# Performance work log

Hardware: AMD Instinct MI355X
Metric: run time of the kernel (lower is better)

The kernel has to match this reference:

```python
import jax, jax.numpy as jnp
import numpy as np

TMPL = jnp.array([[-0.9, 1.2, 0.0], [0.0, 0.0, 0.0], [2.5, 0.0, 0.0]], dtype=jnp.float32)
EYE3 = jnp.eye(3, dtype=jnp.float32)


def _normalize(v, eps=1e-12):
    n = jnp.maximum(jnp.linalg.norm(v, axis=-1, keepdims=True), eps)
    return v / n


def _layer_norm(x, g, b, eps=1e-5):
    mu = jnp.mean(x, axis=-1, keepdims=True)
    var = jnp.var(x, axis=-1, keepdims=True)
    return (x - mu) * jax.lax.rsqrt(var + eps) * g + b


def _build_frames(coords, mask):
    P = coords[..., 0, :]
    C4p = coords[..., 1, :]
    N = coords[..., 2, :]
    e1 = _normalize(N - C4p)
    u = P - C4p
    e2 = _normalize(u - jnp.sum(u * e1, axis=-1, keepdims=True) * e1)
    e3 = jnp.cross(e1, e2)
    R = jnp.stack([e1, e2, e3], axis=-1)  # (B,L,3,3), columns = e1,e2,e3
    pad = ~mask
    R = jnp.where(pad[..., None, None], EYE3, R)
    return R, C4p


def _invariants(R, t):
    # dt[b,i,j] = t[b,j] - t[b,i]
    dt = t[:, None, :, :] - t[:, :, None, :]  # (B,L,L,3)
    # local frame of i: Ri^T @ dt
    dt_l = jnp.einsum('bixk,bijx->bijk', R, dt)  # (B,L,L,3)
    dist = jnp.maximum(jnp.linalg.norm(dt, axis=-1, keepdims=True), 1e-4)
    log_d = jnp.log(dist)
    # trace(Ri^T Rj)
    trace = jnp.einsum('bixk,bjxk->bij', R, R)[..., None]  # (B,L,L,1)
    cos_a = jnp.clip((trace - 1.0) / 2.0, -1.0, 1.0)
    return jnp.concatenate([dist, dt_l, trace, cos_a, log_d], axis=-1)  # (B,L,L,7)


def _skew(v):
    z = jnp.zeros_like(v[..., 0])
    x, y, zz = v[..., 0], v[..., 1], v[..., 2]
    r0 = jnp.stack([z, -zz, y], axis=-1)
    r1 = jnp.stack([zz, z, -x], axis=-1)
    r2 = jnp.stack([-y, x, z], axis=-1)
    return jnp.stack([r0, r1, r2], axis=-2)


def _apply_frame_update(R, t, dr, dt, mask):
    mf = mask.astype(R.dtype)[..., None]
    dr = dr * mf
    dt = dt * mf
    angle = jnp.maximum(jnp.linalg.norm(dr, axis=-1, keepdims=True), 1e-8)
    axis = dr / angle
    cos_a = jnp.cos(angle)[..., None]
    sin_a = jnp.sin(angle)[..., None]
    K = _skew(axis)
    outer = axis[..., :, None] * axis[..., None, :]
    R_delta = cos_a * EYE3 + sin_a * K + (1.0 - cos_a) * outer
    R_new = R_delta @ R
    t_new = t + jnp.einsum('blxy,bly->blx', R, dt)
    return R_new, t_new


def _reconstruct_atoms(R, t):
    # coords[b,l,a,:] = t[b,l] + R[b,l] @ TMPL[a]
    d = jnp.einsum('blxy,ay->blax', R, TMPL)
    return t[:, :, None, :] + d


def _gelu(x):
    return jax.nn.gelu(x, approximate=False)


def _forward(h, coords, mask, pair_w1, pair_b1, pair_w2, pair_b2, gw_w, gw_b, ga_w, ga_b,
             ln_g, ln_b, fh_ln_g, fh_ln_b, fh_w1, fh_b1, fh_w2, fh_b2):
    R, t = _build_frames(coords, mask)
    n_steps = pair_w1.shape[0]
    coords_list = []
    for s in range(n_steps):
        inv = _invariants(R, t)  # (B,L,L,7)
        pm = (mask[:, None, :] & mask[:, :, None]).astype(h.dtype)  # (B,L,L)
        msg = _gelu(inv @ pair_w1[s] + pair_b1[s]) @ pair_w2[s] + pair_b2[s]  # (B,L,L,D)
        n_v = jnp.maximum(jnp.sum(pm, axis=2, keepdims=True), 1.0)  # (B,L,1)
        agg = jnp.sum(msg * pm[..., None], axis=2) / n_v  # (B,L,D)
        h_s = _layer_norm(h, ln_g[s], ln_b[s])
        cat = jnp.concatenate([h_s, agg], axis=-1)
        g = cat @ gw_w[s] + gw_b[s]
        a = jax.nn.sigmoid(cat @ ga_w[s] + ga_b[s])
        h_aug = h + a * g
        fh = _gelu(_layer_norm(h_aug, fh_ln_g, fh_ln_b) @ fh_w1 + fh_b1) @ fh_w2 + fh_b2
        delta_r, delta_t = fh[..., :3], fh[..., 3:]
        R, t = _apply_frame_update(R, t, delta_r, delta_t, mask)
        coords_list.append(_reconstruct_atoms(R, t))
    return coords_list[-1], jnp.stack(coords_list, axis=0)


def setup_inputs() -> dict:
    key = jax.random.key(0)
    B, L, D, H, S = 2, 512, 256, 64, 4
    ks = jax.random.split(key, 16)
    w = lambda k, shp: jax.random.normal(k, shp, dtype=jnp.float32) * 0.02
    return {
        'h': jax.random.normal(ks[0], (B, L, D), dtype=jnp.float32),
        'coords': jax.random.normal(ks[1], (B, L, 3, 3), dtype=jnp.float32),
        'mask': jnp.ones((B, L), dtype=bool),
        'pair_w1': w(ks[2], (S, 7, H)), 'pair_b1': jnp.zeros((S, H), jnp.float32),
        'pair_w2': w(ks[3], (S, H, D)), 'pair_b2': jnp.zeros((S, D), jnp.float32),
        'gw_w': w(ks[4], (S, 2 * D, D)), 'gw_b': jnp.zeros((S, D), jnp.float32),
        'ga_w': w(ks[5], (S, 2 * D, D)), 'ga_b': jnp.zeros((S, D), jnp.float32),
        'ln_g': jnp.ones((S, D), jnp.float32), 'ln_b': jnp.zeros((S, D), jnp.float32),
        'fh_ln_g': jnp.ones((D,), jnp.float32), 'fh_ln_b': jnp.zeros((D,), jnp.float32),
        'fh_w1': w(ks[6], (D, D // 2)), 'fh_b1': jnp.zeros((D // 2,), jnp.float32),
        'fh_w2': w(ks[7], (D // 2, 6)), 'fh_b2': jnp.zeros((6,), jnp.float32),
    }


def reference(h, coords, mask, pair_w1, pair_b1, pair_w2, pair_b2, gw_w, gw_b, ga_w, ga_b,
              ln_g, ln_b, fh_ln_g, fh_ln_b, fh_w1, fh_b1, fh_w2, fh_b2):
    return _forward(h, coords, mask, pair_w1, pair_b1, pair_w2, pair_b2, gw_w, gw_b,
                    ga_w, ga_b, ln_g, ln_b, fh_ln_g, fh_ln_b, fh_w1, fh_b1, fh_w2, fh_b2)
```

## Files before the change

kernel.cpp:

```cpp
#include <hip/hip_runtime.h>
#include <math.h>

#define BB 2
#define LL 512
#define DD 256
#define HH 64
#define NSTEP 4
#define NTOK (BB * LL)

__device__ __forceinline__ float geluf(float x) {
    return 0.5f * x * (1.0f + erff(x * 0.70710678118654752f));
}
__device__ __forceinline__ float sigmoidf_(float x) {
    return 1.0f / (1.0f + expf(-x));
}
__device__ __forceinline__ float gelu_fast(float x) {
    float u = 0.70710678118654752f * x;
    float a = fabsf(u);
    float t = __builtin_amdgcn_rcpf(fmaf(0.3275911f, a, 1.0f));
    float p = fmaf(t, 1.061405429f, -1.453152027f);
    p = fmaf(t, p, 1.421413741f);
    p = fmaf(t, p, -0.284496736f);
    p = fmaf(t, p, 0.254829592f);
    p = p * t;
    float e = __expf(-u * u);
    float erfa = fmaf(-p, e, 1.0f);
    float erfu = copysignf(erfa, u);
    return 0.5f * x * (1.0f + erfu);
}
#define F4C(v, j) ((j) == 0 ? (v).x : (j) == 1 ? (v).y : (j) == 2 ? (v).z : (v).w)

__global__ void build_frames_kernel(const float* __restrict__ coords,
                                    float* __restrict__ Rg, float* __restrict__ tg) {
    int idx = blockIdx.x * blockDim.x + threadIdx.x;
    if (idx >= NTOK) return;
    const float* c = coords + idx * 9;
    float Px = c[0], Py = c[1], Pz = c[2];
    float Cx = c[3], Cy = c[4], Cz = c[5];
    float Nx = c[6], Ny = c[7], Nz = c[8];
    float e1x = Nx - Cx, e1y = Ny - Cy, e1z = Nz - Cz;
    float n1 = fmaxf(sqrtf(e1x * e1x + e1y * e1y + e1z * e1z), 1e-12f);
    e1x /= n1; e1y /= n1; e1z /= n1;
    float ux = Px - Cx, uy = Py - Cy, uz = Pz - Cz;
    float du = ux * e1x + uy * e1y + uz * e1z;
    float e2x = ux - du * e1x, e2y = uy - du * e1y, e2z = uz - du * e1z;
    float n2 = fmaxf(sqrtf(e2x * e2x + e2y * e2y + e2z * e2z), 1e-12f);
    e2x /= n2; e2y /= n2; e2z /= n2;
    float e3x = e1y * e2z - e1z * e2y;
    float e3y = e1z * e2x - e1x * e2z;
    float e3z = e1x * e2y - e1y * e2x;
    float* Rp = Rg + idx * 9;
    Rp[0] = e1x; Rp[1] = e2x; Rp[2] = e3x;
    Rp[3] = e1y; Rp[4] = e2y; Rp[5] = e3y;
    Rp[6] = e1z; Rp[7] = e2z; Rp[8] = e3z;
    tg[idx * 3 + 0] = Cx; tg[idx * 3 + 1] = Cy; tg[idx * 3 + 2] = Cz;
}

__global__ __launch_bounds__(256) void ln4_kernel(
        const float* __restrict__ hIn,
        const float* __restrict__ lng, const float* __restrict__ lnb,
        float* __restrict__ hln) {
    __shared__ float redsh[8];
    const int i = blockIdx.x;
    const int tid = threadIdx.x;
    const int wv = tid >> 6, lane = tid & 63;
    float hv = hIn[(size_t)i * DD + tid];
    float s1 = hv, s2 = hv * hv;
#pragma unroll
    for (int off = 32; off > 0; off >>= 1) {
        s1 += __shfl_xor(s1, off);
        s2 += __shfl_xor(s2, off);
    }
    if (lane == 0) { redsh[wv * 2] = s1; redsh[wv * 2 + 1] = s2; }
    __syncthreads();
    float S1 = redsh[0] + redsh[2] + redsh[4] + redsh[6];
    float S2 = redsh[1] + redsh[3] + redsh[5] + redsh[7];
    float mu = S1 * (1.0f / DD);
    float var = S2 * (1.0f / DD) - mu * mu;
    float rs = rsqrtf(var + 1e-5f);
    float hn = (hv - mu) * rs;
#pragma unroll
    for (int s = 0; s < NSTEP; s++)
        hln[((size_t)s * NTOK + i) * DD + tid] = hn * lng[s * DD + tid] + lnb[s * DD + tid];
}

__global__ void fold_w1_kernel(const float* __restrict__ w1all,
                               const float* __restrict__ b1all,
                               float* __restrict__ w1f) {
    const int s = blockIdx.x;
    const int h = threadIdx.x;
    const float* w1 = w1all + s * 7 * HH;
    float w5 = w1[5 * HH + h];
    float* o = w1f + ((size_t)s * HH + h) * 8;
    o[0] = w1[0 * HH + h];
    o[1] = w1[1 * HH + h];
    o[2] = w1[2 * HH + h];
    o[3] = w1[3 * HH + h];
    o[4] = fmaf(0.5f, w5, w1[4 * HH + h]);
    o[5] = w1[6 * HH + h];
    o[6] = fmaf(-0.5f, w5, b1all[s * HH + h]);
    o[7] = 0.0f;
}

__global__ __launch_bounds__(256) void fuse_w_kernel(
        const float* __restrict__ w2all, const float* __restrict__ b2all,
        const float* __restrict__ gww, const float* __restrict__ gaw,
        const float* __restrict__ gwb, const float* __restrict__ gab,
        float* __restrict__ Wfus, float* __restrict__ biasGA) {
    __shared__ float bsh[256 * 17];

    const int bid = blockIdx.x;
    const int s = bid >> 5;
    const int gate = (bid >> 4) & 1;
    const int ct = bid & 15;
    const int c0 = ct * 16;
    const int tid = threadIdx.x;

    const float* Wb = (gate ? gaw : gww) + (size_t)s * 2 * DD * DD + (size_t)DD * DD;
    {
        const float* src = Wb + (size_t)tid * DD + c0;
        float4 a0 = *(const float4*)(src + 0);
        float4 a1 = *(const float4*)(src + 4);
        float4 a2 = *(const float4*)(src + 8);
        float4 a3 = *(const float4*)(src + 12);
        float* dst = &bsh[tid * 17];
        dst[0] = a0.x; dst[1] = a0.y; dst[2] = a0.z; dst[3] = a0.w;
        dst[4] = a1.x; dst[5] = a1.y; dst[6] = a1.z; dst[7] = a1.w;
        dst[8] = a2.x; dst[9] = a2.y; dst[10] = a2.z; dst[11] = a2.w;
        dst[12] = a3.x; dst[13] = a3.y; dst[14] = a3.z; dst[15] = a3.w;
    }
    __syncthreads();

    const int r = tid & 63;
    const int cg = tid >> 6;
    const float* w2p = w2all + (size_t)s * HH * DD + (size_t)r * DD;
    float4 acc = {0.f, 0.f, 0.f, 0.f};
#pragma unroll 4
    for (int k4 = 0; k4 < 64; k4++) {
        float4 wv = *(const float4*)(w2p + k4 * 4);
#pragma unroll
        for (int j = 0; j < 4; j++) {
            const float* bp = &bsh[(k4 * 4 + j) * 17 + cg * 4];
            float w = F4C(wv, j);
            acc.x = fmaf(w, bp[0], acc.x);
            acc.y = fmaf(w, bp[1], acc.y);
            acc.z = fmaf(w, bp[2], acc.z);
            acc.w = fmaf(w, bp[3], acc.w);
        }
    }
    acc.x *= (1.0f / 512.0f); acc.y *= (1.0f / 512.0f);
    acc.z *= (1.0f / 512.0f); acc.w *= (1.0f / 512.0f);
    *(float4*)&Wfus[((size_t)s * HH + r) * 512 + gate * 256 + c0 + cg * 4] = acc;

    if (tid < 16) {
        const float* b2 = b2all + s * DD;
        float a = 0.0f;
#pragma unroll 4
        for (int m = 0; m < 256; m++) a = fmaf(b2[m], bsh[m * 17 + tid], a);
        const float* gb = (gate ? gab : gwb) + s * DD;
        biasGA[(size_t)s * 512 + gate * 256 + c0 + tid] = a + gb[c0 + tid];
    }
}

__global__ __launch_bounds__(256) void gpreh_kernel(
        const float* __restrict__ hln,
        const float* __restrict__ gww, const float* __restrict__ gaw,
        const float* __restrict__ biasGA,
        float* __restrict__ gpreH) {
    __shared__ float hsh[16 * DD];
    const int bid = blockIdx.x;
    const int s = bid >> 7;
    const int gate = (bid >> 6) & 1;
    const int mt = bid & 63;
    const int tid = threadIdx.x;

    const float* hsrc = hln + ((size_t)s * NTOK + mt * 16) * DD;
    for (int k = tid; k < 16 * DD; k += 256) hsh[k] = hsrc[k];
    __syncthreads();

    const float* W = (gate ? gaw : gww) + (size_t)s * 2 * DD * DD;
    float bias = biasGA[(size_t)s * 512 + gate * 256 + tid];
    float acc[16];
#pragma unroll
    for (int t = 0; t < 16; t++) acc[t] = bias;
#pragma unroll 4
    for (int k = 0; k < DD; k++) {
        float w = W[(size_t)k * DD + tid];
#pragma unroll
        for (int t = 0; t < 16; t++) acc[t] = fmaf(hsh[t * DD + k], w, acc[t]);
    }
    float* out = gpreH + ((size_t)s * NTOK + mt * 16) * 512 + gate * 256 + tid;
#pragma unroll
    for (int t = 0; t < 16; t++) out[(size_t)t * 512] = acc[t];
}

__global__ __launch_bounds__(256, 4) void mega_kernel(
        const float* __restrict__ Rin, const float* __restrict__ tin,
        float* __restrict__ Rout, float* __restrict__ tout,
        const float* __restrict__ w1fS,
        const float* __restrict__ WfusS, const float* __restrict__ gpreHS,
        const float* __restrict__ hIn,
        const float* __restrict__ fhlng, const float* __restrict__ fhlnb,
        const float* __restrict__ fhw1, const float* __restrict__ fhb1,
        const float* __restrict__ fhw2, const float* __restrict__ fhb2,
        float* __restrict__ outFinal, float* __restrict__ outStack, int s) {
    __shared__ float Rsh[LL * 9];
    __shared__ float tsh[LL * 3];
    __shared__ float feats[6][LL];
    __shared__ float asum[HH];
    __shared__ float ln2s[DD];
    __shared__ float fh1p[2 * 128];
    __shared__ float fh1s[128];
    __shared__ float partS[24];
    __shared__ float fhsh[6];
    __shared__ float redsh[8];

    const int i = blockIdx.x;
    const int b = i >> 9;
    const int l = i & (LL - 1);
    const int tid = threadIdx.x;
    const int g = tid >> 6;
    const int hh = tid & 63;

    const float* Rb = Rin + (size_t)b * LL * 9;
    const float* tb = tin + (size_t)b * LL * 3;
    for (int k = tid; k < LL * 9; k += 256) Rsh[k] = Rb[k];
    for (int k = tid; k < LL * 3; k += 256) tsh[k] = tb[k];
    __syncthreads();

    float Ri[9];
#pragma unroll
    for (int k = 0; k < 9; k++) Ri[k] = Rsh[l * 9 + k];
    const float tix = tsh[l * 3 + 0], tiy = tsh[l * 3 + 1], tiz = tsh[l * 3 + 2];

#pragma unroll
    for (int half = 0; half < 2; half++) {
        const int j = half * 256 + tid;
        float dx = tsh[j * 3 + 0] - tix;
        float dy = tsh[j * 3 + 1] - tiy;
        float dz = tsh[j * 3 + 2] - tiz;
        float dl0 = Ri[0] * dx + Ri[3] * dy + Ri[6] * dz;
        float dl1 = Ri[1] * dx + Ri[4] * dy + Ri[7] * dz;
        float dl2 = Ri[2] * dx + Ri[5] * dy + Ri[8] * dz;
        float dist = fmaxf(sqrtf(dx * dx + dy * dy + dz * dz), 1e-4f);
        float tr = 0.0f;
#pragma unroll
        for (int k = 0; k < 9; k++) tr = fmaf(Ri[k], Rsh[j * 9 + k], tr);
        feats[0][j] = dist;
        feats[1][j] = dl0;
        feats[2][j] = dl1;
        feats[3][j] = dl2;
        feats[4][j] = tr;
        feats[5][j] = __logf(dist);
    }
    __syncthreads();

    const int h0g = __builtin_amdgcn_readfirstlane(g) * 16;
#pragma unroll
    for (int hp = 0; hp < 2; hp++) {
        const float* wrow = w1fS + (size_t)(h0g + hp * 8) * 8;
        float acc0 = 0.f, acc1 = 0.f, acc2 = 0.f, acc3 = 0.f;
        float acc4 = 0.f, acc5 = 0.f, acc6 = 0.f, acc7 = 0.f;
        for (int c = 0; c < 8; c++) {
            const int j = c * 64 + hh;
            const float F0 = feats[0][j];
            const float F1 = feats[1][j];
            const float F2 = feats[2][j];
            const float F3 = feats[3][j];
            const float F4 = feats[4][j];
            const float F5 = feats[5][j];
#pragma unroll
            for (int k = 0; k < 8; k++) {
                const float* wr = wrow + k * 8;
                float x = wr[6];
                x = fmaf(F0, wr[0], x);
                x = fmaf(F1, wr[1], x);
                x = fmaf(F2, wr[2], x);
                x = fmaf(F3, wr[3], x);
                x = fmaf(F4, wr[4], x);
                x = fmaf(F5, wr[5], x);
                float gv = gelu_fast(x);
                if (k == 0) acc0 += gv;
                else if (k == 1) acc1 += gv;
                else if (k == 2) acc2 += gv;
                else if (k == 3) acc3 += gv;
                else if (k == 4) acc4 += gv;
                else if (k == 5) acc5 += gv;
                else if (k == 6) acc6 += gv;
                else acc7 += gv;
            }
        }
        float accs[8] = {acc0, acc1, acc2, acc3, acc4, acc5, acc6, acc7};
#pragma unroll
        for (int k = 0; k < 8; k++) {
            float v = accs[k];
#pragma unroll
            for (int off = 1; off < 64; off <<= 1) v += __shfl_xor(v, off);
            if (hh == k) asum[h0g + hp * 8 + k] = v;
        }
    }
    __syncthreads();

    float gpg = gpreHS[(size_t)i * 512 + tid];
    float gpa = gpreHS[(size_t)i * 512 + 256 + tid];
#pragma unroll 8
    for (int k = 0; k < HH; k++) {
        float av = asum[k];
        gpg = fmaf(av, WfusS[(size_t)k * 512 + tid], gpg);
        gpa = fmaf(av, WfusS[(size_t)k * 512 + 256 + tid], gpa);
    }
    float hv = hIn[(size_t)i * DD + tid];
    float haug = hv + sigmoidf_(gpa) * gpg;

    {
        float s1 = haug, s2 = haug * haug;
#pragma unroll
        for (int off = 32; off > 0; off >>= 1) {
            s1 += __shfl_xor(s1, off);
            s2 += __shfl_xor(s2, off);
        }
        if (hh == 0) { redsh[g * 2] = s1; redsh[g * 2 + 1] = s2; }
    }
    __syncthreads();
    {
        float S1 = redsh[0] + redsh[2] + redsh[4] + redsh[6];
        float S2 = redsh[1] + redsh[3] + redsh[5] + redsh[7];
        float mu = S1 * (1.0f / DD);
        float var = S2 * (1.0f / DD) - mu * mu;
        float rs = rsqrtf(var + 1e-5f);
        ln2s[tid] = (haug - mu) * rs * fhlng[tid] + fhlnb[tid];
    }
    __syncthreads();

    {
        const int col = tid & 127;
        const int kh = tid >> 7;
        float a = 0.0f;
        const float* wp = fhw1 + (size_t)(kh * 128) * 128 + col;
        const float* lp = &ln2s[kh * 128];
#pragma unroll 8
        for (int k = 0; k < 128; k++) a = fmaf(lp[k], wp[(size_t)k * 128], a);
        fh1p[kh * 128 + col] = a;
    }
    __syncthreads();
    if (tid < 128) fh1s[tid] = geluf(fh1p[tid] + fh1p[128 + tid] + fhb1[tid]);
    __syncthreads();

    if (tid < 24) {
        const int kq = tid / 6, m = tid % 6;
        float a = 0.0f;
#pragma unroll
        for (int j = 0; j < 32; j++) {
            int k = kq * 32 + j;
            a = fmaf(fh1s[k], fhw2[k * 6 + m], a);
        }
        partS[tid] = a;
    }
    __syncthreads();
    if (tid < 6)
        fhsh[tid] = partS[tid] + partS[6 + tid] + partS[12 + tid] + partS[18 + tid] + fhb2[tid];
    __syncthreads();

    if (tid == 0) {
        float R9[9], t3[3];
#pragma unroll
        for (int k = 0; k < 9; k++) R9[k] = Rsh[l * 9 + k];
        t3[0] = tix; t3[1] = tiy; t3[2] = tiz;
        float drx = fhsh[0], dry = fhsh[1], drz = fhsh[2];
        float dtx = fhsh[3], dty = fhsh[4], dtz = fhsh[5];
        float ang = fmaxf(sqrtf(drx * drx + dry * dry + drz * drz), 1e-8f);
        float ax = drx / ang, ay = dry / ang, az = drz / ang;
        float ca = cosf(ang), sa = sinf(ang), omc = 1.0f - ca;
        float Rd[9];
        Rd[0] = ca + omc * ax * ax;        Rd[1] = -sa * az + omc * ax * ay;  Rd[2] = sa * ay + omc * ax * az;
        Rd[3] = sa * az + omc * ay * ax;   Rd[4] = ca + omc * ay * ay;        Rd[5] = -sa * ax + omc * ay * az;
        Rd[6] = -sa * ay + omc * az * ax;  Rd[7] = sa * ax + omc * az * ay;   Rd[8] = ca + omc * az * az;
        float Rn[9];
#pragma unroll
        for (int x = 0; x < 3; x++)
#pragma unroll
            for (int y = 0; y < 3; y++)
                Rn[x * 3 + y] = Rd[x * 3 + 0] * R9[0 * 3 + y]
                              + Rd[x * 3 + 1] * R9[1 * 3 + y]
                              + Rd[x * 3 + 2] * R9[2 * 3 + y];
        float tn[3];
#pragma unroll
        for (int x = 0; x < 3; x++)
            tn[x] = t3[x] + R9[x * 3 + 0] * dtx + R9[x * 3 + 1] * dty + R9[x * 3 + 2] * dtz;
#pragma unroll
        for (int k = 0; k < 9; k++) Rout[(size_t)i * 9 + k] = Rn[k];
#pragma unroll
        for (int k = 0; k < 3; k++) tout[(size_t)i * 3 + k] = tn[k];
        float* os = outStack + ((size_t)s * NTOK + i) * 9;
        float av[9];
#pragma unroll
        for (int x = 0; x < 3; x++) {
            float r0 = Rn[x * 3 + 0], r1 = Rn[x * 3 + 1];
            av[0 * 3 + x] = tn[x] - 0.9f * r0 + 1.2f * r1;
            av[1 * 3 + x] = tn[x];
            av[2 * 3 + x] = tn[x] + 2.5f * r0;
        }
#pragma unroll
        for (int k = 0; k < 9; k++) os[k] = av[k];
        if (s == NSTEP - 1) {
            float* of = outFinal + (size_t)i * 9;
#pragma unroll
            for (int k = 0; k < 9; k++) of[k] = av[k];
        }
    }
}

extern "C" void kernel_launch(void* const* d_in, const int* in_sizes, int n_in,
                              void* d_out, int out_size, void* d_ws, size_t ws_size,
                              hipStream_t stream) {
    const float* h      = (const float*)d_in[0];
    const float* coords = (const float*)d_in[1];
    const float* pw1   = (const float*)d_in[3];
    const float* pb1   = (const float*)d_in[4];
    const float* pw2   = (const float*)d_in[5];
    const float* pb2   = (const float*)d_in[6];
    const float* gww   = (const float*)d_in[7];
    const float* gwb   = (const float*)d_in[8];
    const float* gaw   = (const float*)d_in[9];
    const float* gab   = (const float*)d_in[10];
    const float* lng   = (const float*)d_in[11];
    const float* lnb   = (const float*)d_in[12];
    const float* fhlng = (const float*)d_in[13];
    const float* fhlnb = (const float*)d_in[14];
    const float* fhw1  = (const float*)d_in[15];
    const float* fhb1  = (const float*)d_in[16];
    const float* fhw2  = (const float*)d_in[17];
    const float* fhb2  = (const float*)d_in[18];

    float* ws     = (float*)d_ws;
    float* R0     = ws;
    float* t0     = ws + 9216;
    float* R1     = ws + 12288;
    float* t1     = ws + 21504;
    float* hln    = ws + 24576;
    float* gpreH  = ws + 24576 + 1048576;
    float* Wfus   = ws + 24576 + 1048576 + 2097152;
    float* biasGA = ws + 24576 + 1048576 + 2097152 + 131072;
    float* w1f    = ws + 24576 + 1048576 + 2097152 + 131072 + 2048;

    float* outFinal = (float*)d_out;
    float* outStack = outFinal + NTOK * 9;

    build_frames_kernel<<<NTOK / 256, 256, 0, stream>>>(coords, R0, t0);
    ln4_kernel<<<NTOK, 256, 0, stream>>>(h, lng, lnb, hln);
    fold_w1_kernel<<<NSTEP, 64, 0, stream>>>(pw1, pb1, w1f);
    fuse_w_kernel<<<128, 256, 0, stream>>>(pw2, pb2, gww, gaw, gwb, gab, Wfus, biasGA);
    gpreh_kernel<<<512, 256, 0, stream>>>(hln, gww, gaw, biasGA, gpreH);

    for (int s = 0; s < NSTEP; s++) {
        const float* Rin = (s & 1) ? R1 : R0;
        const float* tin = (s & 1) ? t1 : t0;
        float* Rout = (s & 1) ? R0 : R1;
        float* tout = (s & 1) ? t0 : t1;
        mega_kernel<<<NTOK, 256, 0, stream>>>(
            Rin, tin, Rout, tout,
            w1f + (size_t)s * HH * 8,
            Wfus + (size_t)s * HH * 512, gpreH + (size_t)s * NTOK * 512,
            h, fhlng, fhlnb, fhw1, fhb1, fhw2, fhb2,
            outFinal, outStack, s);
    }
}
```

Before: 214.8 us.

## Split mega kernel into pair kernel and batched 8-token epilogue kernel

The per-token mega kernel is split in two. A pair kernel computes the pairwise GELU sums and writes them to global memory. A separate epilogue kernel then handles 8 tokens per 512-thread block, so each weight load for the Wfus, fhw1 and fhw2 matvecs is reused across 8 tokens instead of being reloaded per token. The pair kernel also sheds its large epilogue shared-memory and register footprint, which may help occupancy. The cost is an extra kernel launch per step and a global round-trip for the sums.

New measurement: 280.3 us. +30.5%, slower.

```diff
diff --git a/kernel.cpp b/kernel.cpp
--- a/kernel.cpp
+++ b/kernel.cpp
@@ -194,26 +194,13 @@
     for (int t = 0; t < 16; t++) out[(size_t)t * 512] = acc[t];
 }
 
-__global__ __launch_bounds__(256, 4) void mega_kernel(
+__global__ __launch_bounds__(256, 4) void pair_kernel(
         const float* __restrict__ Rin, const float* __restrict__ tin,
-        float* __restrict__ Rout, float* __restrict__ tout,
         const float* __restrict__ w1fS,
-        const float* __restrict__ WfusS, const float* __restrict__ gpreHS,
-        const float* __restrict__ hIn,
-        const float* __restrict__ fhlng, const float* __restrict__ fhlnb,
-        const float* __restrict__ fhw1, const float* __restrict__ fhb1,
-        const float* __restrict__ fhw2, const float* __restrict__ fhb2,
-        float* __restrict__ outFinal, float* __restrict__ outStack, int s) {
+        float* __restrict__ asumG) {
     __shared__ float Rsh[LL * 9];
     __shared__ float tsh[LL * 3];
     __shared__ float feats[6][LL];
-    __shared__ float asum[HH];
-    __shared__ float ln2s[DD];
-    __shared__ float fh1p[2 * 128];
-    __shared__ float fh1s[128];
-    __shared__ float partS[24];
-    __shared__ float fhsh[6];
-    __shared__ float redsh[8];
 
     const int i = blockIdx.x;
     const int b = i >> 9;
@@ -296,78 +283,149 @@
             float v = accs[k];
 #pragma unroll
             for (int off = 1; off < 64; off <<= 1) v += __shfl_xor(v, off);
-            if (hh == k) asum[h0g + hp * 8 + k] = v;
-        }
-    }
-    __syncthreads();
-
-    float gpg = gpreHS[(size_t)i * 512 + tid];
-    float gpa = gpreHS[(size_t)i * 512 + 256 + tid];
-#pragma unroll 8
-    for (int k = 0; k < HH; k++) {
-        float av = asum[k];
-        gpg = fmaf(av, WfusS[(size_t)k * 512 + tid], gpg);
-        gpa = fmaf(av, WfusS[(size_t)k * 512 + 256 + tid], gpa);
-    }
-    float hv = hIn[(size_t)i * DD + tid];
-    float haug = hv + sigmoidf_(gpa) * gpg;
+            if (hh == k) asumG[(size_t)i * HH + h0g + hp * 8 + k] = v;
+        }
+    }
+}
+
+__global__ __launch_bounds__(512) void epi_kernel(
+        const float* __restrict__ Rin, const float* __restrict__ tin,
+        float* __restrict__ Rout, float* __restrict__ tout,
+        const float* __restrict__ asumG,
+        const float* __restrict__ WfusS, const float* __restrict__ gpreHS,
+        const float* __restrict__ hIn,
+        const float* __restrict__ fhlng, const float* __restrict__ fhlnb,
+        const float* __restrict__ fhw1, const float* __restrict__ fhb1,
+        const float* __restrict__ fhw2, const float* __restrict__ fhb2,
+        float* __restrict__ outFinal, float* __restrict__ outStack, int s) {
+    __shared__ float ash[8][HH];
+    __shared__ float gg[8][256];
+    __shared__ float ga[8][256];
+    __shared__ float ln2[8][256];
+    __shared__ float fh1[8][128];
+    __shared__ float partS[8][24];
+    __shared__ float fhsh[8][6];
+    __shared__ float red2[2][4][4][2];
+
+    const int i0 = blockIdx.x * 8;
+    const int tid = threadIdx.x;
+
+    ash[tid >> 6][tid & 63] = asumG[(size_t)i0 * HH + tid];
+    __syncthreads();
 
     {
-        float s1 = haug, s2 = haug * haug;
+        const int c = tid & 255;
+        const int gate = tid >> 8;
+        const float* wp = WfusS + gate * 256 + c;
+        float acc[8];
+#pragma unroll
+        for (int t = 0; t < 8; t++) acc[t] = 0.0f;
+#pragma unroll 4
+        for (int k = 0; k < HH; k++) {
+            float w = wp[(size_t)k * 512];
+#pragma unroll
+            for (int t = 0; t < 8; t++) acc[t] = fmaf(ash[t][k], w, acc[t]);
+        }
+        float* dst = gate ? &ga[0][0] : &gg[0][0];
+#pragma unroll
+        for (int t = 0; t < 8; t++)
+            dst[t * 256 + c] = acc[t] + gpreHS[(size_t)(i0 + t) * 512 + gate * 256 + c];
+    }
+    __syncthreads();
+
+    const int d = tid & 255;
+    const int tp = tid >> 8;
+    const int wv = tid >> 6;
+    const int wvg = wv & 3;
+    const int lane = tid & 63;
+    float haug[4];
+#pragma unroll
+    for (int tt = 0; tt < 4; tt++) {
+        int t = tp * 4 + tt;
+        float hv = hIn[(size_t)(i0 + t) * DD + d];
+        haug[tt] = hv + sigmoidf_(ga[t][d]) * gg[t][d];
+    }
+    {
+        float s1[4], s2[4];
+#pragma unroll
+        for (int tt = 0; tt < 4; tt++) { s1[tt] = haug[tt]; s2[tt] = haug[tt] * haug[tt]; }
 #pragma unroll
         for (int off = 32; off > 0; off >>= 1) {
-            s1 += __shfl_xor(s1, off);
-            s2 += __shfl_xor(s2, off);
-        }
-        if (hh == 0) { redsh[g * 2] = s1; redsh[g * 2 + 1] = s2; }
+#pragma unroll
+            for (int tt = 0; tt < 4; tt++) {
+                s1[tt] += __shfl_xor(s1[tt], off);
+                s2[tt] += __shfl_xor(s2[tt], off);
+            }
+        }
+        if (lane == 0) {
+#pragma unroll
+            for (int tt = 0; tt < 4; tt++) {
+                red2[tp][tt][wvg][0] = s1[tt];
+                red2[tp][tt][wvg][1] = s2[tt];
+            }
+        }
     }
     __syncthreads();
     {
-        float S1 = redsh[0] + redsh[2] + redsh[4] + redsh[6];
-        float S2 = redsh[1] + redsh[3] + redsh[5] + redsh[7];
-        float mu = S1 * (1.0f / DD);
-        float var = S2 * (1.0f / DD) - mu * mu;
-        float rs = rsqrtf(var + 1e-5f);
-        ln2s[tid] = (haug - mu) * rs * fhlng[tid] + fhlnb[tid];
+        float gv = fhlng[d], bv = fhlnb[d];
+#pragma unroll
+        for (int tt = 0; tt < 4; tt++) {
+            float S1 = red2[tp][tt][0][0] + red2[tp][tt][1][0] + red2[tp][tt][2][0] + red2[tp][tt][3][0];
+            float S2 = red2[tp][tt][0][1] + red2[tp][tt][1][1] + red2[tp][tt][2][1] + red2[tp][tt][3][1];
+            float mu = S1 * (1.0f / DD);
+            float var = S2 * (1.0f / DD) - mu * mu;
+            float rs = rsqrtf(var + 1e-5f);
+            ln2[tp * 4 + tt][d] = (haug[tt] - mu) * rs * gv + bv;
+        }
     }
     __syncthreads();
 
     {
-        const int col = tid & 127;
-        const int kh = tid >> 7;
-        float a = 0.0f;
-        const float* wp = fhw1 + (size_t)(kh * 128) * 128 + col;
-        const float* lp = &ln2s[kh * 128];
-#pragma unroll 8
-        for (int k = 0; k < 128; k++) a = fmaf(lp[k], wp[(size_t)k * 128], a);
-        fh1p[kh * 128 + col] = a;
-    }
-    __syncthreads();
-    if (tid < 128) fh1s[tid] = geluf(fh1p[tid] + fh1p[128 + tid] + fhb1[tid]);
-    __syncthreads();
-
-    if (tid < 24) {
-        const int kq = tid / 6, m = tid % 6;
+        const int tok = tid >> 6;
+        const int c2 = (tid & 63) * 2;
+        float a0 = fhb1[c2], a1 = fhb1[c2 + 1];
+        const float* lp = &ln2[tok][0];
+#pragma unroll 4
+        for (int k = 0; k < DD; k++) {
+            float lv = lp[k];
+            float2 w2v = *(const float2*)&fhw1[(size_t)k * 128 + c2];
+            a0 = fmaf(lv, w2v.x, a0);
+            a1 = fmaf(lv, w2v.y, a1);
+        }
+        fh1[tok][c2] = geluf(a0);
+        fh1[tok][c2 + 1] = geluf(a1);
+    }
+    __syncthreads();
+
+    if (tid < 192) {
+        const int t = tid / 24, rem = tid % 24;
+        const int m = rem >> 2, kq = rem & 3;
         float a = 0.0f;
 #pragma unroll
         for (int j = 0; j < 32; j++) {
             int k = kq * 32 + j;
-            a = fmaf(fh1s[k], fhw2[k * 6 + m], a);
-        }
-        partS[tid] = a;
-    }
-    __syncthreads();
-    if (tid < 6)
-        fhsh[tid] = partS[tid] + partS[6 + tid] + partS[12 + tid] + partS[18 + tid] + fhb2[tid];
-    __syncthreads();
-
-    if (tid == 0) {
+            a = fmaf(fh1[t][k], fhw2[k * 6 + m], a);
+        }
+        partS[t][m * 4 + kq] = a;
+    }
+    __syncthreads();
+    if (tid < 48) {
+        const int t = tid / 6, m = tid % 6;
+        fhsh[t][m] = partS[t][m * 4 + 0] + partS[t][m * 4 + 1]
+                   + partS[t][m * 4 + 2] + partS[t][m * 4 + 3] + fhb2[m];
+    }
+    __syncthreads();
+
+    if (tid < 8) {
+        const int t = tid;
+        const int i = i0 + t;
         float R9[9], t3[3];
 #pragma unroll
-        for (int k = 0; k < 9; k++) R9[k] = Rsh[l * 9 + k];
-        t3[0] = tix; t3[1] = tiy; t3[2] = tiz;
-        float drx = fhsh[0], dry = fhsh[1], drz = fhsh[2];
-        float dtx = fhsh[3], dty = fhsh[4], dtz = fhsh[5];
+        for (int k = 0; k < 9; k++) R9[k] = Rin[(size_t)i * 9 + k];
+#pragma unroll
+        for (int k = 0; k < 3; k++) t3[k] = tin[(size_t)i * 3 + k];
+        float drx = fhsh[t][0], dry = fhsh[t][1], drz = fhsh[t][2];
+        float dtx = fhsh[t][3], dty = fhsh[t][4], dtz = fhsh[t][5];
         float ang = fmaxf(sqrtf(drx * drx + dry * dry + drz * drz), 1e-8f);
         float ax = drx / ang, ay = dry / ang, az = drz / ang;
         float ca = cosf(ang), sa = sinf(ang), omc = 1.0f - ca;
@@ -442,6 +500,7 @@
     float* Wfus   = ws + 24576 + 1048576 + 2097152;
     float* biasGA = ws + 24576 + 1048576 + 2097152 + 131072;
     float* w1f    = ws + 24576 + 1048576 + 2097152 + 131072 + 2048;
+    float* asumG  = ws + 24576 + 1048576 + 2097152 + 131072 + 2048 + 2048;
 
     float* outFinal = (float*)d_out;
     float* outStack = outFinal + NTOK * 9;
@@ -457,9 +516,10 @@
         const float* tin = (s & 1) ? t1 : t0;
         float* Rout = (s & 1) ? R0 : R1;
         float* tout = (s & 1) ? t0 : t1;
-        mega_kernel<<<NTOK, 256, 0, stream>>>(
-            Rin, tin, Rout, tout,
-            w1f + (size_t)s * HH * 8,
+        pair_kernel<<<NTOK, 256, 0, stream>>>(
+            Rin, tin, w1f + (size_t)s * HH * 8, asumG);
+        epi_kernel<<<NTOK / 8, 512, 0, stream>>>(
+            Rin, tin, Rout, tout, asumG,
             Wfus + (size_t)s * HH * 512, gpreH + (size_t)s * NTOK * 512,
             h, fhlng, fhlnb, fhw1, fhb1, fhw2, fhb2,
             outFinal, outStack, s);
```
